# Kernel tuning notes

Measured on AMD Instinct MI355X. Metric: run time of the kernel, lower is better.

The kernel has to match this reference:

```python
import jax, jax.numpy as jnp
import numpy as np

BN_EPS = 1e-5


def setup_inputs() -> dict:
    key = jax.random.key(0)
    ks = jax.random.split(key, 13)
    B, Ct, H, W = 2, 64, 32, 32
    Co, E = 32, 64
    Ho, Wo = 3 * H, 3 * W
    s = 0.05
    return {
        "x_thermal": jax.random.normal(ks[0], (B, Ct, H, W), jnp.float32),
        "x_optical": jax.random.normal(ks[1], (B, Co, Ho, Wo), jnp.float32),
        # 1x1 conv weights stored as [out_c, in_c]
        "q_w": jax.random.normal(ks[2], (E, Ct), jnp.float32) * s,
        "q_b": jax.random.normal(ks[3], (E,), jnp.float32) * s,
        "k_w": jax.random.normal(ks[4], (E, Co), jnp.float32) * s,
        "k_b": jax.random.normal(ks[5], (E,), jnp.float32) * s,
        "v_w": jax.random.normal(ks[6], (Co, Co), jnp.float32) * s,
        "v_b": jax.random.normal(ks[7], (Co,), jnp.float32) * s,
        # out ConvBlock: 1x1 conv (no bias) -> BatchNorm (eval, running stats) -> ReLU
        "out_w": jax.random.normal(ks[8], (Ct, Co), jnp.float32) * s,
        "bn_gamma": jnp.ones((Ct,), jnp.float32) + jax.random.normal(ks[9], (Ct,), jnp.float32) * 0.01,
        "bn_beta": jax.random.normal(ks[10], (Ct,), jnp.float32) * 0.01,
        "bn_mean": jax.random.normal(ks[11], (Ct,), jnp.float32) * 0.01,
        "bn_var": jax.random.uniform(ks[12], (Ct,), jnp.float32, 0.5, 1.5),
    }


def reference(x_thermal, x_optical, q_w, q_b, k_w, k_b, v_w, v_b,
              out_w, bn_gamma, bn_beta, bn_mean, bn_var):
    B, Co, Ho, Wo = x_optical.shape
    N = Ho * Wo
    # F.interpolate(mode='bilinear', align_corners=False) == jax.image.resize 'bilinear' (half-pixel)
    x_up = jax.image.resize(x_thermal, (B, x_thermal.shape[1], Ho, Wo), method="bilinear")
    # 1x1 conv projections
    q = (jnp.einsum("bchw,ec->behw", x_up, q_w) + q_b[None, :, None, None]).reshape(B, -1, N)
    k = (jnp.einsum("bchw,ec->behw", x_optical, k_w) + k_b[None, :, None, None]).reshape(B, -1, N)
    v = (jnp.einsum("bchw,oc->bohw", x_optical, v_w) + v_b[None, :, None, None]).reshape(B, -1, N)
    E = q.shape[1]
    # attn[b, n, m] = sum_e q[b,e,n] * k[b,e,m]  (full N x N score matrix)
    scores = jnp.einsum("ben,bem->bnm", q, k) / jnp.sqrt(jnp.asarray(E, q.dtype))
    attn = jax.nn.softmax(scores, axis=-1)
    # out = v @ attn^T : out[b,o,n] = sum_m v[b,o,m] * attn[b,n,m]
    out = jnp.einsum("bom,bnm->bon", v, attn).reshape(B, Co, Ho, Wo)
    # out ConvBlock: 1x1 conv (bias=False) -> BatchNorm (eval) -> ReLU
    g = jnp.einsum("bchw,tc->bthw", out, out_w)
    g = (g - bn_mean[None, :, None, None]) * (bn_gamma / jnp.sqrt(bn_var + BN_EPS))[None, :, None, None] \
        + bn_beta[None, :, None, None]
    return jax.nn.relu(g)
```

## Files before the change

kernel.cpp:

```cpp
#include <hip/hip_runtime.h>
#include <hip/hip_bf16.h>


constexpr int B   = 2;
constexpr int N   = 9216;
constexpr int E   = 64;
constexpr int CO  = 32;
constexpr int CT  = 64;
constexpr int KVBLK = 64;

constexpr int KV_BLKS = (B * N) / 128;
constexpr int QS_BLKS = (B * 1024) / 128;

typedef _Float16 f16x8 __attribute__((ext_vector_type(8)));
typedef _Float16 f16x4 __attribute__((ext_vector_type(4)));
typedef float    f32x4 __attribute__((ext_vector_type(4)));
typedef unsigned int u32;

#define MFMA(a, b, c) __builtin_amdgcn_mfma_f32_16x16x32_f16((a), (b), (c), 0, 0, 0)

#define GLOAD16(gsrc, ldst)                                                     \
  __builtin_amdgcn_global_load_lds(                                             \
      (const __attribute__((address_space(1))) u32*)(gsrc),                     \
      (__attribute__((address_space(3))) u32*)(ldst), 16, 0, 0)

#define PKRTZ(a, b) __builtin_bit_cast(unsigned, __builtin_amdgcn_cvt_pkrtz((a), (b)))

#define SC 0.18033688011112042f

__global__ __launch_bounds__(256) void proj_gemm_kernel(
    const float* __restrict__ xo,
    const float* __restrict__ kw, const float* __restrict__ kb,
    const float* __restrict__ vw, const float* __restrict__ vb,
    _Float16* __restrict__ K, _Float16* __restrict__ Vt,
    const float* __restrict__ xt,
    const float* __restrict__ qw, const float* __restrict__ qb,
    float* __restrict__ Qs)
{
  __shared__ u32 Xl[128 * 32];

  const int tid  = threadIdx.x;
  const int wave = tid >> 6, lane = tid & 63;
  const int r16  = lane & 15, g = lane >> 4;
  const int bid  = blockIdx.x;

  if (bid < KV_BLKS) {
    const int p0 = bid * 128;
    const int b  = p0 / N, n0 = p0 % N;

    {
      const int p  = tid & 127;
      const int ch = tid >> 7;
#pragma unroll
      for (int cc = 0; cc < 8; ++cc) {
        const int c = cc * 4 + ch * 2;
        const float x0 = xo[((size_t)b * CO + c) * N + n0 + p];
        const float x1 = xo[((size_t)b * CO + c + 1) * N + n0 + p];
        Xl[p * 16 + ((c >> 1) ^ (p & 15))] = PKRTZ(x0, x1);
      }
    }
    __syncthreads();

    f16x8 xb[2];
#pragma unroll
    for (int pt = 0; pt < 2; ++pt) {
      const int p = (wave * 2 + pt) * 16 + r16;
      union { u32 u[4]; f16x8 v; } fr;
#pragma unroll
      for (int j = 0; j < 4; ++j)
        fr.u[j] = Xl[p * 16 + ((g * 4 + j) ^ r16)];
      xb[pt] = fr.v;
    }

#pragma unroll
    for (int et = 0; et < 4; ++et) {
      const float* kwe = kw + (size_t)(et * 16 + r16) * 32 + g * 8;
      const f32x4 w0 = *(const f32x4*)(kwe);
      const f32x4 w1 = *(const f32x4*)(kwe + 4);
      union { u32 u[4]; f16x8 v; } af;
      af.u[0] = PKRTZ(w0[0], w0[1]); af.u[1] = PKRTZ(w0[2], w0[3]);
      af.u[2] = PKRTZ(w1[0], w1[1]); af.u[3] = PKRTZ(w1[2], w1[3]);

      const int e0 = et * 16 + 4 * g;
      const float b0 = kb[e0], b1 = kb[e0 + 1], b2 = kb[e0 + 2], b3 = kb[e0 + 3];
#pragma unroll
      for (int pt = 0; pt < 2; ++pt) {
        f32x4 d = (f32x4){0.f, 0.f, 0.f, 0.f};
        d = MFMA(af.v, xb[pt], d);
        const int p = p0 + (wave * 2 + pt) * 16 + r16;
        uint2 pk;
        pk.x = PKRTZ(d[0] + b0, d[1] + b1);
        pk.y = PKRTZ(d[2] + b2, d[3] + b3);
        *(uint2*)(K + (size_t)p * E + e0) = pk;
      }
    }

#pragma unroll
    for (int ot = 0; ot < 2; ++ot) {
      const float* vwo = vw + (size_t)(ot * 16 + r16) * 32 + g * 8;
      const f32x4 w0 = *(const f32x4*)(vwo);
      const f32x4 w1 = *(const f32x4*)(vwo + 4);
      union { u32 u[4]; f16x8 v; } af;
      af.u[0] = PKRTZ(w0[0], w0[1]); af.u[1] = PKRTZ(w0[2], w0[3]);
      af.u[2] = PKRTZ(w1[0], w1[1]); af.u[3] = PKRTZ(w1[2], w1[3]);

      const int o0 = ot * 16 + 4 * g;
      const float b0 = vb[o0], b1 = vb[o0 + 1], b2 = vb[o0 + 2], b3 = vb[o0 + 3];
#pragma unroll
      for (int pt = 0; pt < 2; ++pt) {
        f32x4 d = (f32x4){0.f, 0.f, 0.f, 0.f};
        d = MFMA(af.v, xb[pt], d);
        const int n = n0 + (wave * 2 + pt) * 16 + r16;
        Vt[((size_t)b * CO + o0)     * N + n] = (_Float16)(d[0] + b0);
        Vt[((size_t)b * CO + o0 + 1) * N + n] = (_Float16)(d[1] + b1);
        Vt[((size_t)b * CO + o0 + 2) * N + n] = (_Float16)(d[2] + b2);
        Vt[((size_t)b * CO + o0 + 3) * N + n] = (_Float16)(d[3] + b3);
      }
    }
  } else {
    const int qbid = bid - KV_BLKS;
    const int qp0  = qbid * 128;
    const int b    = qp0 >> 10, p10 = qp0 & 1023;

    {
      const int p  = tid & 127;
      const int ch = tid >> 7;
#pragma unroll
      for (int cc = 0; cc < 16; ++cc) {
        const int c = cc * 4 + ch * 2;
        const float x0 = xt[(((size_t)b * 64 + c) << 10) + p10 + p];
        const float x1 = xt[(((size_t)b * 64 + c + 1) << 10) + p10 + p];
        Xl[p * 32 + ((c >> 1) ^ (p & 31))] = PKRTZ(x0, x1);
      }
    }
    __syncthreads();

    f16x8 xb[2][2];
#pragma unroll
    for (int pt = 0; pt < 2; ++pt) {
      const int pl = (wave * 2 + pt) * 16 + r16;
#pragma unroll
      for (int ks = 0; ks < 2; ++ks) {
        union { u32 u[4]; f16x8 v; } fr;
#pragma unroll
        for (int j = 0; j < 4; ++j)
          fr.u[j] = Xl[pl * 32 + ((ks * 16 + g * 4 + j) ^ (pl & 31))];
        xb[pt][ks] = fr.v;
      }
    }

#pragma unroll
    for (int et = 0; et < 4; ++et) {
      union { u32 u[4]; f16x8 v; } af[2];
#pragma unroll
      for (int ks = 0; ks < 2; ++ks) {
        const float* qwe = qw + (size_t)(et * 16 + r16) * 64 + ks * 32 + g * 8;
        const f32x4 w0 = *(const f32x4*)(qwe);
        const f32x4 w1 = *(const f32x4*)(qwe + 4);
        af[ks].u[0] = PKRTZ(w0[0], w0[1]); af[ks].u[1] = PKRTZ(w0[2], w0[3]);
        af[ks].u[2] = PKRTZ(w1[0], w1[1]); af[ks].u[3] = PKRTZ(w1[2], w1[3]);
      }

      const int e0 = et * 16 + 4 * g;
      const f32x4 qb4 = {qb[e0], qb[e0 + 1], qb[e0 + 2], qb[e0 + 3]};
#pragma unroll
      for (int pt = 0; pt < 2; ++pt) {
        f32x4 d = (f32x4){0.f, 0.f, 0.f, 0.f};
        d = MFMA(af[0].v, xb[pt][0], d);
        d = MFMA(af[1].v, xb[pt][1], d);
        const int pix = qp0 + (wave * 2 + pt) * 16 + r16;
        *(f32x4*)(Qs + (size_t)pix * 64 + e0) = (d + qb4) * SC;
      }
    }
  }
}

__global__ __launch_bounds__(256) void upsample_q_kernel(
    const float* __restrict__ Qs,
    _Float16* __restrict__ Q)
{
  const int tid = blockIdx.x * 256 + threadIdx.x;
  const int p   = tid >> 2;
  const int eq  = tid & 3;
  const int b   = p / N, n = p % N;
  const int ho  = n / 96, wo = n % 96;

  const float sh = (ho + 0.5f) * (1.0f / 3.0f) - 0.5f;
  const float sw = (wo + 0.5f) * (1.0f / 3.0f) - 0.5f;
  int h0 = (int)floorf(sh); const float fh = sh - (float)h0;
  int w0 = (int)floorf(sw); const float fw = sw - (float)w0;
  int h1 = min(h0 + 1, 31); h0 = max(h0, 0);
  int w1 = min(w0 + 1, 31); w0 = max(w0, 0);

  const float c00 = (1.f - fh) * (1.f - fw), c01 = (1.f - fh) * fw;
  const float c10 = fh * (1.f - fw),         c11 = fh * fw;

  const float* Qb = Qs + (size_t)b * 1024 * 64 + eq * 16;
  const f32x4* q00 = (const f32x4*)(Qb + (h0 * 32 + w0) * 64);
  const f32x4* q01 = (const f32x4*)(Qb + (h0 * 32 + w1) * 64);
  const f32x4* q10 = (const f32x4*)(Qb + (h1 * 32 + w0) * 64);
  const f32x4* q11 = (const f32x4*)(Qb + (h1 * 32 + w1) * 64);

  union { _Float16 h[16]; uint4 v[2]; } pk;
#pragma unroll
  for (int j4 = 0; j4 < 4; ++j4) {
    const f32x4 a = q00[j4] * c00 + q01[j4] * c01 + q10[j4] * c10 + q11[j4] * c11;
#pragma unroll
    for (int i = 0; i < 4; ++i) pk.h[4 * j4 + i] = (_Float16)a[i];
  }

  _Float16* Qp = Q + (size_t)p * E + eq * 16;
  *(uint4*)(Qp)     = pk.v[0];
  *(uint4*)(Qp + 8) = pk.v[1];
}

template<int SPLIT>
__global__ __launch_bounds__(256) void attn_kernel(
    const _Float16* __restrict__ Q,
    const _Float16* __restrict__ K,
    const _Float16* __restrict__ Vt,
    _Float16* __restrict__ OutWS,
    float* __restrict__ SumWS)
{
  constexpr int MCHUNK = N / SPLIT;
  constexpr int ROUNDS = MCHUNK / KVBLK;

  __shared__ _Float16 Kl[2][KVBLK][64];
  __shared__ _Float16 Vl[2][CO][KVBLK];

  const int tid  = threadIdx.x;
  const int wave = tid >> 6, lane = tid & 63;
  const int r16  = lane & 15, g = lane >> 4;

  const int work  = blockIdx.x;
  const int chunk = work & (SPLIT - 1);
  const int t128  = work / SPLIT;
  const int b     = t128 / 72;
  const int rowbase = (t128 % 72) * 128 + wave * 32;

  const _Float16* Qb = Q  + ((size_t)b * N + rowbase) * E;
  const _Float16* Kb = K  + (size_t)b * N * E;
  const _Float16* Vb = Vt + (size_t)b * CO * N;

  const int sub = lane >> 3, c8 = lane & 7;
  const int swz = 8 * (c8 ^ sub);

  const int mstart = chunk * MCHUNK;

  f16x8 qf[2][2];
#pragma unroll
  for (int rt = 0; rt < 2; ++rt)
#pragma unroll
    for (int ks = 0; ks < 2; ++ks)
      qf[rt][ks] = *(const f16x8*)(Qb + (rt * 16 + r16) * E + ks * 32 + g * 8);

  f16x8 onesf;
#pragma unroll
  for (int i = 0; i < 8; ++i) onesf[i] = (_Float16)1.0f;

  {
    const _Float16* gk = Kb + (size_t)(mstart + 16 * wave + sub) * E + swz;
    GLOAD16(gk,         &Kl[0][16 * wave][0]);
    GLOAD16(gk + 8 * E, &Kl[0][16 * wave + 8][0]);
    const _Float16* gv = Vb + (size_t)(8 * wave + sub) * N + mstart + swz;
    GLOAD16(gv,         &Vl[0][8 * wave][0]);
  }

  f32x4 oacc[2][2];
#pragma unroll
  for (int a = 0; a < 2; ++a)
#pragma unroll
    for (int c = 0; c < 2; ++c) oacc[a][c] = (f32x4){0.f, 0.f, 0.f, 0.f};
  f32x4 sacc[2];
  sacc[0] = (f32x4){0.f, 0.f, 0.f, 0.f};
  sacc[1] = (f32x4){0.f, 0.f, 0.f, 0.f};

  const int rsw   = (r16 & 7) << 4;
  const int kcol0 = ((0 * 64 + g * 16) ^ rsw) >> 1;
  const int kcol1 = ((1 * 64 + g * 16) ^ rsw) >> 1;

  __syncthreads();

  int cur = 0;
  for (int r = 0; r < ROUNDS; ++r) {
    if (r + 1 < ROUNDS) {
      const int m0 = mstart + (r + 1) * KVBLK;
      const _Float16* gk = Kb + (size_t)(m0 + 16 * wave + sub) * E + swz;
      GLOAD16(gk,         &Kl[cur ^ 1][16 * wave][0]);
      GLOAD16(gk + 8 * E, &Kl[cur ^ 1][16 * wave + 8][0]);
      const _Float16* gv = Vb + (size_t)(8 * wave + sub) * N + m0 + swz;
      GLOAD16(gv,         &Vl[cur ^ 1][8 * wave][0]);
    }

#pragma unroll
    for (int it = 0; it < 2; ++it) {
      f16x8 kf[2][2];
#pragma unroll
      for (int mt = 0; mt < 2; ++mt) {
        const int krow = it * 32 + mt * 16 + r16;
        kf[mt][0] = *(const f16x8*)&Kl[cur][krow][kcol0];
        kf[mt][1] = *(const f16x8*)&Kl[cur][krow][kcol1];
      }
      union { f16x4 h[2]; f16x8 v; } vf[2];
#pragma unroll
      for (int ot = 0; ot < 2; ++ot) {
        const int vrow = ot * 16 + r16;
        const int v0 = ((it * 64 + 8 * g) ^ rsw) >> 1;
        const int v1 = ((it * 64 + 32 + 8 * g) ^ rsw) >> 1;
        vf[ot].h[0] = *(const f16x4*)&Vl[cur][vrow][v0];
        vf[ot].h[1] = *(const f16x4*)&Vl[cur][vrow][v1];
      }

#pragma unroll
      for (int rt = 0; rt < 2; ++rt) {
        f32x4 s0 = (f32x4){0.f, 0.f, 0.f, 0.f};
        f32x4 s1 = (f32x4){0.f, 0.f, 0.f, 0.f};
        s0 = MFMA(kf[0][0], qf[rt][0], s0);
        s0 = MFMA(kf[0][1], qf[rt][1], s0);
        s1 = MFMA(kf[1][0], qf[rt][0], s1);
        s1 = MFMA(kf[1][1], qf[rt][1], s1);

        float p0[4], p1[4];
#pragma unroll
        for (int i = 0; i < 4; ++i) {
          p0[i] = __builtin_amdgcn_exp2f(s0[i]);
          p1[i] = __builtin_amdgcn_exp2f(s1[i]);
        }

        union { unsigned u[4]; f16x8 v; } pb;
        pb.u[0] = PKRTZ(p0[0], p0[1]);
        pb.u[1] = PKRTZ(p0[2], p0[3]);
        pb.u[2] = PKRTZ(p1[0], p1[1]);
        pb.u[3] = PKRTZ(p1[2], p1[3]);

        oacc[rt][0] = MFMA(vf[0].v, pb.v, oacc[rt][0]);
        oacc[rt][1] = MFMA(vf[1].v, pb.v, oacc[rt][1]);
        sacc[rt]    = MFMA(onesf,   pb.v, sacc[rt]);
      }
    }

    __syncthreads();
    cur ^= 1;
  }

  _Float16* OW = OutWS + (size_t)(chunk * B + b) * N * CO;
  float*    SW = SumWS + (size_t)(chunk * B + b) * N;
#pragma unroll
  for (int rt = 0; rt < 2; ++rt) {
    const int n = rowbase + rt * 16 + r16;
    if (g == 0) SW[n] = sacc[rt][0];
#pragma unroll
    for (int ot = 0; ot < 2; ++ot) {
      uint2 pko;
      pko.x = PKRTZ(oacc[rt][ot][0], oacc[rt][ot][1]);
      pko.y = PKRTZ(oacc[rt][ot][2], oacc[rt][ot][3]);
      *(uint2*)(OW + (size_t)n * CO + ot * 16 + 4 * g) = pko;
    }
  }
}

template<int SPLIT>
__global__ __launch_bounds__(256) void epi_kernel(
    const _Float16* __restrict__ OutWS, const float* __restrict__ SumWS,
    const float* __restrict__ ow, const float* __restrict__ gamma,
    const float* __restrict__ beta, const float* __restrict__ mean,
    const float* __restrict__ var, float* __restrict__ out)
{
  __shared__ float part[4][64][33];
  __shared__ float psum[4][64];

  const int tid  = threadIdx.x;
  const int nloc = tid & 63, grp = tid >> 6;
  const int pix  = blockIdx.x * 64 + nloc;
  const int b    = pix / N, n = pix % N;

  float accf[32];
#pragma unroll
  for (int j = 0; j < 32; ++j) accf[j] = 0.f;
  float ssum = 0.f;
#pragma unroll
  for (int k = 0; k < SPLIT / 4; ++k) {
    const int sc = grp * (SPLIT / 4) + k;
    const f16x8* src = (const f16x8*)(OutWS + ((size_t)(sc * B + b) * N + n) * CO);
#pragma unroll
    for (int j = 0; j < 4; ++j) {
      const f16x8 c = src[j];
#pragma unroll
      for (int i = 0; i < 8; ++i) accf[j * 8 + i] += (float)c[i];
    }
    ssum += SumWS[(size_t)(sc * B + b) * N + n];
  }
#pragma unroll
  for (int j = 0; j < 32; ++j) part[grp][nloc][j] = accf[j];
  psum[grp][nloc] = ssum;
  __syncthreads();

  const float s = psum[0][nloc] + psum[1][nloc] + psum[2][nloc] + psum[3][nloc];
  const float inv = 1.f / s;
  float onr[CO];
#pragma unroll
  for (int o = 0; o < CO; ++o)
    onr[o] = (part[0][nloc][o] + part[1][nloc][o] +
              part[2][nloc][o] + part[3][nloc][o]) * inv;

#pragma unroll
  for (int i = 0; i < 16; ++i) {
    const int t = grp + 4 * i;
    float acc2 = 0.f;
#pragma unroll
    for (int o = 0; o < CO; ++o) acc2 += onr[o] * ow[t * CO + o];
    const float scl = gamma[t] * rsqrtf(var[t] + 1e-5f);
    const float bia = beta[t] - mean[t] * scl;
    const float gv  = acc2 * scl + bia;
    out[(size_t)(b * CT + t) * N + n] = fmaxf(gv, 0.f);
  }
}

extern "C" void kernel_launch(void* const* d_in, const int* in_sizes, int n_in,
                              void* d_out, int out_size, void* d_ws, size_t ws_size,
                              hipStream_t stream) {
  const float* xt = (const float*)d_in[0];
  const float* xo = (const float*)d_in[1];
  const float* qw = (const float*)d_in[2];
  const float* qb = (const float*)d_in[3];
  const float* kw = (const float*)d_in[4];
  const float* kb = (const float*)d_in[5];
  const float* vw = (const float*)d_in[6];
  const float* vb = (const float*)d_in[7];
  const float* ow = (const float*)d_in[8];
  const float* gm = (const float*)d_in[9];
  const float* bt = (const float*)d_in[10];
  const float* mn = (const float*)d_in[11];
  const float* vr = (const float*)d_in[12];

  char* ws = (char*)d_ws;
  _Float16* Qd  = (_Float16*)ws;  ws += (size_t)B * N * E * 2;
  _Float16* Kd  = (_Float16*)ws;  ws += (size_t)B * N * E * 2;
  _Float16* Vtd = (_Float16*)ws;  ws += (size_t)B * CO * N * 2;
  float* Qs     = (float*)ws;     ws += (size_t)B * 1024 * 64 * 4;
  _Float16* OutWS = (_Float16*)ws;
  const size_t base   = (size_t)(ws - (char*)d_ws);
  const size_t need16 = base + (size_t)16 * B * N * (CO * 2 + 4);

  proj_gemm_kernel<<<KV_BLKS + QS_BLKS, 256, 0, stream>>>(
      xo, kw, kb, vw, vb, Kd, Vtd, xt, qw, qb, Qs);
  upsample_q_kernel<<<(B * N * 4) / 256, 256, 0, stream>>>(Qs, Qd);

  if (ws_size >= need16) {
    float* SumWS = (float*)(OutWS + (size_t)16 * B * N * CO);
    attn_kernel<16><<<(N / 128) * B * 16, 256, 0, stream>>>(Qd, Kd, Vtd, OutWS, SumWS);
    epi_kernel<16><<<(B * N) / 64, 256, 0, stream>>>(OutWS, SumWS, ow, gm, bt, mn, vr,
                                                     (float*)d_out);
  } else {
    float* SumWS = (float*)(OutWS + (size_t)8 * B * N * CO);
    attn_kernel<8><<<(N / 128) * B * 8, 256, 0, stream>>>(Qd, Kd, Vtd, OutWS, SumWS);
    epi_kernel<8><<<(B * N) / 64, 256, 0, stream>>>(OutWS, SumWS, ow, gm, bt, mn, vr,
                                                    (float*)d_out);
  }
}
```

Before: 146.2 us.

## Fuse Q upsampling and split-K epilogue into attention kernel via atomic counter

Folds the bilinear upsample of Q into the attention kernel's Q-fragment load, so the full-resolution fp16 Q buffer and its separate kernel go away. It also replaces the separate epilogue kernel with a last-block-done pattern. Each tile increments an atomic counter, and the final split block reduces the partial outputs, applies the 1x1 conv, BatchNorm and ReLU, and writes the result. Two launches and a round trip of Q through global memory are removed. In exchange the kernel adds a memset, atomic synchronisation, and a serial tail in which one block per tile does the whole epilogue with 128 active pixels per block.

```diff
diff --git a/kernel.cpp b/kernel.cpp
--- a/kernel.cpp
+++ b/kernel.cpp
@@ -175,58 +175,24 @@
   }
 }
 
-__global__ __launch_bounds__(256) void upsample_q_kernel(
+template<int SPLIT>
+__global__ __launch_bounds__(256) void attn_fused_kernel(
     const float* __restrict__ Qs,
-    _Float16* __restrict__ Q)
-{
-  const int tid = blockIdx.x * 256 + threadIdx.x;
-  const int p   = tid >> 2;
-  const int eq  = tid & 3;
-  const int b   = p / N, n = p % N;
-  const int ho  = n / 96, wo = n % 96;
-
-  const float sh = (ho + 0.5f) * (1.0f / 3.0f) - 0.5f;
-  const float sw = (wo + 0.5f) * (1.0f / 3.0f) - 0.5f;
-  int h0 = (int)floorf(sh); const float fh = sh - (float)h0;
-  int w0 = (int)floorf(sw); const float fw = sw - (float)w0;
-  int h1 = min(h0 + 1, 31); h0 = max(h0, 0);
-  int w1 = min(w0 + 1, 31); w0 = max(w0, 0);
-
-  const float c00 = (1.f - fh) * (1.f - fw), c01 = (1.f - fh) * fw;
-  const float c10 = fh * (1.f - fw),         c11 = fh * fw;
-
-  const float* Qb = Qs + (size_t)b * 1024 * 64 + eq * 16;
-  const f32x4* q00 = (const f32x4*)(Qb + (h0 * 32 + w0) * 64);
-  const f32x4* q01 = (const f32x4*)(Qb + (h0 * 32 + w1) * 64);
-  const f32x4* q10 = (const f32x4*)(Qb + (h1 * 32 + w0) * 64);
-  const f32x4* q11 = (const f32x4*)(Qb + (h1 * 32 + w1) * 64);
-
-  union { _Float16 h[16]; uint4 v[2]; } pk;
-#pragma unroll
-  for (int j4 = 0; j4 < 4; ++j4) {
-    const f32x4 a = q00[j4] * c00 + q01[j4] * c01 + q10[j4] * c10 + q11[j4] * c11;
-#pragma unroll
-    for (int i = 0; i < 4; ++i) pk.h[4 * j4 + i] = (_Float16)a[i];
-  }
-
-  _Float16* Qp = Q + (size_t)p * E + eq * 16;
-  *(uint4*)(Qp)     = pk.v[0];
-  *(uint4*)(Qp + 8) = pk.v[1];
-}
-
-template<int SPLIT>
-__global__ __launch_bounds__(256) void attn_kernel(
-    const _Float16* __restrict__ Q,
     const _Float16* __restrict__ K,
     const _Float16* __restrict__ Vt,
+    const float* __restrict__ ow, const float* __restrict__ gm,
+    const float* __restrict__ bt, const float* __restrict__ mn,
+    const float* __restrict__ vr, float* __restrict__ out,
     _Float16* __restrict__ OutWS,
-    float* __restrict__ SumWS)
+    float* __restrict__ SumWS,
+    unsigned* __restrict__ ctr)
 {
   constexpr int MCHUNK = N / SPLIT;
   constexpr int ROUNDS = MCHUNK / KVBLK;
 
   __shared__ _Float16 Kl[2][KVBLK][64];
   __shared__ _Float16 Vl[2][CO][KVBLK];
+  __shared__ int lastflag;
 
   const int tid  = threadIdx.x;
   const int wave = tid >> 6, lane = tid & 63;
@@ -238,7 +204,6 @@
   const int b     = t128 / 72;
   const int rowbase = (t128 % 72) * 128 + wave * 32;
 
-  const _Float16* Qb = Q  + ((size_t)b * N + rowbase) * E;
   const _Float16* Kb = K  + (size_t)b * N * E;
   const _Float16* Vb = Vt + (size_t)b * CO * N;
 
@@ -248,11 +213,41 @@
   const int mstart = chunk * MCHUNK;
 
   f16x8 qf[2][2];
-#pragma unroll
-  for (int rt = 0; rt < 2; ++rt)
-#pragma unroll
-    for (int ks = 0; ks < 2; ++ks)
-      qf[rt][ks] = *(const f16x8*)(Qb + (rt * 16 + r16) * E + ks * 32 + g * 8);
+  {
+    const float* Qbase = Qs + ((size_t)b << 16);
+#pragma unroll
+    for (int rt = 0; rt < 2; ++rt) {
+      const int n  = rowbase + rt * 16 + r16;
+      const int ho = n / 96, wo = n % 96;
+      const float sh = (ho + 0.5f) * (1.0f / 3.0f) - 0.5f;
+      const float sw = (wo + 0.5f) * (1.0f / 3.0f) - 0.5f;
+      int h0 = (int)floorf(sh); const float fh = sh - (float)h0;
+      int w0 = (int)floorf(sw); const float fw = sw - (float)w0;
+      int h1 = min(h0 + 1, 31); h0 = max(h0, 0);
+      int w1 = min(w0 + 1, 31); w0 = max(w0, 0);
+      const float c00 = (1.f - fh) * (1.f - fw), c01 = (1.f - fh) * fw;
+      const float c10 = fh * (1.f - fw),         c11 = fh * fw;
+      const float* p00 = Qbase + (h0 * 32 + w0) * 64;
+      const float* p01 = Qbase + (h0 * 32 + w1) * 64;
+      const float* p10 = Qbase + (h1 * 32 + w0) * 64;
+      const float* p11 = Qbase + (h1 * 32 + w1) * 64;
+#pragma unroll
+      for (int ks = 0; ks < 2; ++ks) {
+        union { u32 u[4]; f16x8 v; } qa;
+#pragma unroll
+        for (int j4 = 0; j4 < 2; ++j4) {
+          const int e0 = ks * 32 + g * 8 + j4 * 4;
+          const f32x4 a = *(const f32x4*)(p00 + e0) * c00
+                        + *(const f32x4*)(p01 + e0) * c01
+                        + *(const f32x4*)(p10 + e0) * c10
+                        + *(const f32x4*)(p11 + e0) * c11;
+          qa.u[j4 * 2]     = PKRTZ(a[0], a[1]);
+          qa.u[j4 * 2 + 1] = PKRTZ(a[2], a[3]);
+        }
+        qf[rt][ks] = qa.v;
+      }
+    }
+  }
 
   f16x8 onesf;
 #pragma unroll
@@ -357,62 +352,48 @@
       *(uint2*)(OW + (size_t)n * CO + ot * 16 + 4 * g) = pko;
     }
   }
-}
-
-template<int SPLIT>
-__global__ __launch_bounds__(256) void epi_kernel(
-    const _Float16* __restrict__ OutWS, const float* __restrict__ SumWS,
-    const float* __restrict__ ow, const float* __restrict__ gamma,
-    const float* __restrict__ beta, const float* __restrict__ mean,
-    const float* __restrict__ var, float* __restrict__ out)
-{
-  __shared__ float part[4][64][33];
-  __shared__ float psum[4][64];
-
-  const int tid  = threadIdx.x;
-  const int nloc = tid & 63, grp = tid >> 6;
-  const int pix  = blockIdx.x * 64 + nloc;
-  const int b    = pix / N, n = pix % N;
-
-  float accf[32];
-#pragma unroll
-  for (int j = 0; j < 32; ++j) accf[j] = 0.f;
-  float ssum = 0.f;
-#pragma unroll
-  for (int k = 0; k < SPLIT / 4; ++k) {
-    const int sc = grp * (SPLIT / 4) + k;
-    const f16x8* src = (const f16x8*)(OutWS + ((size_t)(sc * B + b) * N + n) * CO);
-#pragma unroll
-    for (int j = 0; j < 4; ++j) {
-      const f16x8 c = src[j];
-#pragma unroll
-      for (int i = 0; i < 8; ++i) accf[j * 8 + i] += (float)c[i];
-    }
-    ssum += SumWS[(size_t)(sc * B + b) * N + n];
-  }
-#pragma unroll
-  for (int j = 0; j < 32; ++j) part[grp][nloc][j] = accf[j];
-  psum[grp][nloc] = ssum;
+
   __syncthreads();
-
-  const float s = psum[0][nloc] + psum[1][nloc] + psum[2][nloc] + psum[3][nloc];
-  const float inv = 1.f / s;
-  float onr[CO];
-#pragma unroll
-  for (int o = 0; o < CO; ++o)
-    onr[o] = (part[0][nloc][o] + part[1][nloc][o] +
-              part[2][nloc][o] + part[3][nloc][o]) * inv;
-
-#pragma unroll
-  for (int i = 0; i < 16; ++i) {
-    const int t = grp + 4 * i;
-    float acc2 = 0.f;
-#pragma unroll
-    for (int o = 0; o < CO; ++o) acc2 += onr[o] * ow[t * CO + o];
-    const float scl = gamma[t] * rsqrtf(var[t] + 1e-5f);
-    const float bia = beta[t] - mean[t] * scl;
-    const float gv  = acc2 * scl + bia;
-    out[(size_t)(b * CT + t) * N + n] = fmaxf(gv, 0.f);
+  if (tid == 0) {
+    const unsigned old = __hip_atomic_fetch_add(&ctr[t128], 1u,
+                              __ATOMIC_ACQ_REL, __HIP_MEMORY_SCOPE_AGENT);
+    lastflag = (old == (unsigned)(SPLIT - 1));
+  }
+  __syncthreads();
+
+  if (lastflag) {
+    const int nloc = tid & 127;
+    const int th   = tid >> 7;
+    const int n    = (t128 % 72) * 128 + nloc;
+
+    float accf[CO];
+#pragma unroll
+    for (int o = 0; o < CO; ++o) accf[o] = 0.f;
+    float ssum = 0.f;
+#pragma unroll 4
+    for (int sc = 0; sc < SPLIT; ++sc) {
+      const f16x8* src = (const f16x8*)(OutWS + ((size_t)(sc * B + b) * N + n) * CO);
+#pragma unroll
+      for (int j = 0; j < 4; ++j) {
+        const f16x8 c = src[j];
+#pragma unroll
+        for (int i = 0; i < 8; ++i) accf[j * 8 + i] += (float)c[i];
+      }
+      ssum += SumWS[(size_t)(sc * B + b) * N + n];
+    }
+    const float inv = 1.f / ssum;
+
+#pragma unroll 1
+    for (int i = 0; i < 32; ++i) {
+      const int t = th * 32 + i;
+      float acc2 = 0.f;
+#pragma unroll
+      for (int o = 0; o < CO; ++o) acc2 += accf[o] * ow[t * CO + o];
+      const float scl = gm[t] * rsqrtf(vr[t] + 1e-5f);
+      const float bia = bt[t] - mn[t] * scl;
+      const float gv  = acc2 * inv * scl + bia;
+      out[(size_t)(b * CT + t) * N + n] = fmaxf(gv, 0.f);
+    }
   }
 }
 
@@ -434,7 +415,7 @@
   const float* vr = (const float*)d_in[12];
 
   char* ws = (char*)d_ws;
-  _Float16* Qd  = (_Float16*)ws;  ws += (size_t)B * N * E * 2;
+  unsigned* ctr = (unsigned*)ws;  ws += 1024;
   _Float16* Kd  = (_Float16*)ws;  ws += (size_t)B * N * E * 2;
   _Float16* Vtd = (_Float16*)ws;  ws += (size_t)B * CO * N * 2;
   float* Qs     = (float*)ws;     ws += (size_t)B * 1024 * 64 * 4;
@@ -442,19 +423,17 @@
   const size_t base   = (size_t)(ws - (char*)d_ws);
   const size_t need16 = base + (size_t)16 * B * N * (CO * 2 + 4);
 
+  hipMemsetAsync(ctr, 0, 1024, stream);
   proj_gemm_kernel<<<KV_BLKS + QS_BLKS, 256, 0, stream>>>(
       xo, kw, kb, vw, vb, Kd, Vtd, xt, qw, qb, Qs);
-  upsample_q_kernel<<<(B * N * 4) / 256, 256, 0, stream>>>(Qs, Qd);
 
   if (ws_size >= need16) {
     float* SumWS = (float*)(OutWS + (size_t)16 * B * N * CO);
-    attn_kernel<16><<<(N / 128) * B * 16, 256, 0, stream>>>(Qd, Kd, Vtd, OutWS, SumWS);
-    epi_kernel<16><<<(B * N) / 64, 256, 0, stream>>>(OutWS, SumWS, ow, gm, bt, mn, vr,
-                                                     (float*)d_out);
+    attn_fused_kernel<16><<<(N / 128) * B * 16, 256, 0, stream>>>(
+        Qs, Kd, Vtd, ow, gm, bt, mn, vr, (float*)d_out, OutWS, SumWS, ctr);
   } else {
     float* SumWS = (float*)(OutWS + (size_t)8 * B * N * CO);
-    attn_kernel<8><<<(N / 128) * B * 8, 256, 0, stream>>>(Qd, Kd, Vtd, OutWS, SumWS);
-    epi_kernel<8><<<(B * N) / 64, 256, 0, stream>>>(OutWS, SumWS, ow, gm, bt, mn, vr,
-                                                    (float*)d_out);
+    attn_fused_kernel<8><<<(N / 128) * B * 8, 256, 0, stream>>>(
+        Qs, Kd, Vtd, ow, gm, bt, mn, vr, (float*)d_out, OutWS, SumWS, ctr);
   }
 }
```

Measured after the change: 265.1 us. +81.3%, slower.
